# Kernel optimization log

Hardware: AMD Instinct MI355X
Metric: run time of the kernel (lower is better)

## Reference

```python
import jax, jax.numpy as jnp
import numpy as np

WEIGHT = 0.1
SELF_WEIGHT = 1.0
OTHER_WEIGHT = 1.0

def setup_inputs() -> dict:
    key = jax.random.key(0)
    k1, k2 = jax.random.split(key)
    B, D = 8192, 128
    output = jax.random.normal(k1, (B, D), dtype=jnp.float32)
    target = jax.random.normal(k2, (B, D), dtype=jnp.float32)
    return {"output": output, "target": target}

def reference(output, target):
    # Pairwise Euclidean distances d[i, n] = ||output[i] - target[n]||_2
    # no [B, B, D] intermediate).
    B = output.shape[0]
    xx = jnp.sum(output * output, axis=-1)          # [B]
    yy = jnp.sum(target * target, axis=-1)          # [B]
    d2 = xx[:, None] + yy[None, :] - 2.0 * (output @ target.T)  # [B, B]
    d = jnp.sqrt(jnp.maximum(d2, 0.0))
    diag_sum = jnp.trace(d)                          # sum of self distances
    total_sum = jnp.sum(d)
    other_sum = total_sum - diag_sum
    loss = (-diag_sum * SELF_WEIGHT + other_sum * OTHER_WEIGHT) / B * WEIGHT
    return loss
```

## Files before the change

### kernel.cpp

```cpp
#include <hip/hip_runtime.h>
#include <stdint.h>

typedef float f32x16 __attribute__((ext_vector_type(16)));
typedef int v8i __attribute__((ext_vector_type(8)));
typedef int v4i __attribute__((ext_vector_type(4)));

#define BDIM 8192


__global__ __launch_bounds__(256) void prep_kernel(const float* __restrict__ out_f,
                                                   const float* __restrict__ tgt_f,
                                                   uint8_t* __restrict__ ak,
                                                   float* __restrict__ xxyy) {
    const float* src = blockIdx.y ? tgt_f : out_f;
    uint8_t* dst = ak + (size_t)blockIdx.y * (1u << 20);
    float* nrm = xxyy + (size_t)blockIdx.y * BDIM;

    const int tid = threadIdx.x;
    const int lane = tid & 63;
    const int w = tid >> 6;
    const int jg = lane & 15;
    const int r = blockIdx.x * 16 + w * 4 + (lane >> 4);

    const float4* s4 = (const float4*)(src + (size_t)r * 128 + jg * 8);
    float4 a = s4[0], b = s4[1];

    uint32_t w0 = __builtin_amdgcn_cvt_pk_fp8_f32(a.x, a.y, 0, false);
    w0 = __builtin_amdgcn_cvt_pk_fp8_f32(a.z, a.w, w0, true);
    uint32_t w1 = __builtin_amdgcn_cvt_pk_fp8_f32(b.x, b.y, 0, false);
    w1 = __builtin_amdgcn_cvt_pk_fp8_f32(b.z, b.w, w1, true);

    *(uint2*)(dst + (jg >> 3) * 524288 + ((jg >> 2) & 1) * 262144
                  + ((jg >> 1) & 1) * 131072 + r * 16 + (jg & 1) * 8)
        = make_uint2(w0, w1);

    float sq = a.x*a.x + a.y*a.y + a.z*a.z + a.w*a.w
             + b.x*b.x + b.y*b.y + b.z*b.z + b.w*b.w;
    sq += __shfl_xor(sq, 1); sq += __shfl_xor(sq, 2);
    sq += __shfl_xor(sq, 4); sq += __shfl_xor(sq, 8);
    if (jg == 0) nrm[r] = sq;
}

__global__ __launch_bounds__(256, 4) void dist_kernel(const uint8_t* __restrict__ Ak,
                                                      const uint8_t* __restrict__ Bk,
                                                      const float* __restrict__ xxg,
                                                      const float* __restrict__ yyg,
                                                      float* __restrict__ partials) {
    __shared__ uint8_t sA[16384] __attribute__((aligned(16)));
    __shared__ uint8_t sB[16384] __attribute__((aligned(16)));
    __shared__ float xxl[128];
    __shared__ float yyl[128];
    __shared__ float wsum[4];

    const int tid = threadIdx.x;
    const int lane = tid & 63;
    const int wid = tid >> 6;
    const int wr = wid >> 1, wc = wid & 1;
    const int bx = blockIdx.x, by = blockIdx.y;

    {
        const int c0 = wid * 8;
        #pragma unroll
        for (int i = 0; i < 8; ++i) {
            int c = c0 + i;
            int mat = c >> 4, rem = c & 15, s = rem >> 1, half = rem & 1;
            int bidx = mat ? by : bx;
            const uint8_t* g = (mat ? Bk : Ak)
                + (s >> 2) * 524288 + ((s >> 1) & 1) * 262144 + (s & 1) * 131072
                + ((size_t)(bidx * 128 + half * 64)) * 16 + lane * 16;
            uint8_t* l = (mat ? sB : sA) + s * 2048 + half * 1024;
            __builtin_amdgcn_global_load_lds(
                (const __attribute__((address_space(1))) unsigned int*)g,
                (__attribute__((address_space(3))) unsigned int*)l, 16, 0, 0);
        }
    }
    if (tid < 128) xxl[tid] = xxg[bx * 128 + tid];
    else           yyl[tid - 128] = yyg[by * 128 + (tid - 128)];
    __syncthreads();

    const int lm = lane & 31;
    const int fh = lane >> 5;
    const v4i* A4 = (const v4i*)sA;
    const v4i* B4 = (const v4i*)sB;

    f32x16 acc[2][2] = {};
    #pragma unroll
    for (int S = 0; S < 2; ++S) {
        const int sb = S * 4 + fh * 2;
        v4i a0l = A4[(sb + 0) * 128 + wr * 64 + lm];
        v4i a0h = A4[(sb + 1) * 128 + wr * 64 + lm];
        v4i a1l = A4[(sb + 0) * 128 + wr * 64 + 32 + lm];
        v4i a1h = A4[(sb + 1) * 128 + wr * 64 + 32 + lm];
        v4i b0l = B4[(sb + 0) * 128 + wc * 64 + lm];
        v4i b0h = B4[(sb + 1) * 128 + wc * 64 + lm];
        v4i b1l = B4[(sb + 0) * 128 + wc * 64 + 32 + lm];
        v4i b1h = B4[(sb + 1) * 128 + wc * 64 + 32 + lm];
        v8i a0 = __builtin_shufflevector(a0l, a0h, 0, 1, 2, 3, 4, 5, 6, 7);
        v8i a1 = __builtin_shufflevector(a1l, a1h, 0, 1, 2, 3, 4, 5, 6, 7);
        v8i b0 = __builtin_shufflevector(b0l, b0h, 0, 1, 2, 3, 4, 5, 6, 7);
        v8i b1 = __builtin_shufflevector(b1l, b1h, 0, 1, 2, 3, 4, 5, 6, 7);
        acc[0][0] = __builtin_amdgcn_mfma_scale_f32_32x32x64_f8f6f4(
                        a0, b0, acc[0][0], 0, 0, 0, 0x7F7F7F7F, 0, 0x7F7F7F7F);
        acc[0][1] = __builtin_amdgcn_mfma_scale_f32_32x32x64_f8f6f4(
                        a0, b1, acc[0][1], 0, 0, 0, 0x7F7F7F7F, 0, 0x7F7F7F7F);
        acc[1][0] = __builtin_amdgcn_mfma_scale_f32_32x32x64_f8f6f4(
                        a1, b0, acc[1][0], 0, 0, 0, 0x7F7F7F7F, 0, 0x7F7F7F7F);
        acc[1][1] = __builtin_amdgcn_mfma_scale_f32_32x32x64_f8f6f4(
                        a1, b1, acc[1][1], 0, 0, 0, 0x7F7F7F7F, 0, 0x7F7F7F7F);
    }

    float s0 = 0.0f, s1 = 0.0f;
    #pragma unroll
    for (int tr = 0; tr < 2; ++tr) {
        float xv[16];
        #pragma unroll
        for (int q = 0; q < 4; ++q) {
            float4 t = *(const float4*)&xxl[wr * 64 + tr * 32 + 8 * q + 4 * fh];
            xv[q * 4 + 0] = t.x; xv[q * 4 + 1] = t.y;
            xv[q * 4 + 2] = t.z; xv[q * 4 + 3] = t.w;
        }
        #pragma unroll
        for (int tc = 0; tc < 2; ++tc) {
            float yv = yyl[wc * 64 + tc * 32 + lm];
            #pragma unroll
            for (int r = 0; r < 16; ++r) {
                float d2 = fmaf(-2.0f, acc[tr][tc][r], xv[r] + yv);
                float d = __builtin_amdgcn_sqrtf(__builtin_fabsf(d2));
                if (r & 1) s1 += d; else s0 += d;
            }
        }
    }
    float s = s0 + s1;

    if (bx == by && wr == wc) {
        #pragma unroll
        for (int t = 0; t < 2; ++t) {
            #pragma unroll
            for (int r = 0; r < 16; ++r) {
                int row = (r & 3) + 8 * (r >> 2) + 4 * fh;
                if (row == lm) {
                    int idx = wr * 64 + t * 32 + row;
                    float d2 = fmaf(-2.0f, acc[t][t][r], xxl[idx] + yyl[idx]);
                    s -= 2.0f * __builtin_amdgcn_sqrtf(__builtin_fabsf(d2));
                }
            }
        }
    }

    #pragma unroll
    for (int off = 32; off > 0; off >>= 1) s += __shfl_down(s, off);
    if (lane == 0) wsum[wid] = s;
    __syncthreads();
    if (tid == 0) partials[by * 64 + bx] = wsum[0] + wsum[1] + wsum[2] + wsum[3];
}

__global__ __launch_bounds__(256) void reduce_kernel(const float* __restrict__ partials,
                                                     float* __restrict__ out) {
    __shared__ float wsum[4];
    float s = 0.0f;
    #pragma unroll
    for (int i = 0; i < 16; ++i) s += partials[threadIdx.x + i * 256];
    #pragma unroll
    for (int off = 32; off > 0; off >>= 1) s += __shfl_down(s, off);
    int lane = threadIdx.x & 63, wid = threadIdx.x >> 6;
    if (lane == 0) wsum[wid] = s;
    __syncthreads();
    if (threadIdx.x == 0)
        out[0] = (wsum[0] + wsum[1] + wsum[2] + wsum[3]) * (0.1f / 8192.0f);
}

extern "C" void kernel_launch(void* const* d_in, const int* in_sizes, int n_in,
                              void* d_out, int out_size, void* d_ws, size_t ws_size,
                              hipStream_t stream) {
    const float* output = (const float*)d_in[0];
    const float* target = (const float*)d_in[1];

    uint8_t* ws = (uint8_t*)d_ws;
    uint8_t* ak      = ws;
    float*   xxyy    = (float*)(ws + (2u << 20));
    float*   partial = (float*)(ws + (2u << 20) + (64u << 10));

    prep_kernel<<<dim3(512, 2), 256, 0, stream>>>(output, target, ak, xxyy);
    dist_kernel<<<dim3(64, 64), 256, 0, stream>>>(ak, ak + (1u << 20),
                                                  xxyy, xxyy + BDIM, partial);
    reduce_kernel<<<1, 256, 0, stream>>>(partial, (float*)d_out);
}
```

Measured before the change: 78.58 us.

## Loop each block over four B tiles with double-buffered async LDS staging

Each distance block now keeps its A tile resident and iterates over four consecutive B column tiles. The next B tile and its norms are prefetched into a second LDS buffer while the current tile is computed. This amortizes the A load and launch cost and overlaps global-to-LDS transfers with MFMA work, cutting the grid from 4096 to 1024 blocks and the partial count to match. The costs are a larger LDS footprint (occupancy hint lowered to 3), fewer blocks to fill the GPU, and an extra barrier per iteration.

```diff
diff --git a/kernel.cpp b/kernel.cpp
--- a/kernel.cpp
+++ b/kernel.cpp
@@ -41,117 +41,148 @@
     if (jg == 0) nrm[r] = sq;
 }
 
-__global__ __launch_bounds__(256, 4) void dist_kernel(const uint8_t* __restrict__ Ak,
+__device__ __forceinline__ size_t seg_off(int s) {
+    return (size_t)(s >> 2) * 524288 + (size_t)((s >> 1) & 1) * 262144
+         + (size_t)(s & 1) * 131072;
+}
+
+__device__ __forceinline__ void stage_tile(const uint8_t* g0, int r0,
+                                           uint8_t* dst, int wid, int lane) {
+    #pragma unroll
+    for (int i = 0; i < 4; ++i) {
+        int c = wid * 4 + i;
+        int s = c >> 1, half = c & 1;
+        const uint8_t* g = g0 + seg_off(s) + (size_t)(r0 + half * 64 + lane) * 16;
+        uint8_t* l = dst + s * 2048 + half * 1024 + lane * 16;
+        __builtin_amdgcn_global_load_lds(
+            (const __attribute__((address_space(1))) unsigned int*)g,
+            (__attribute__((address_space(3))) unsigned int*)l, 16, 0, 0);
+    }
+}
+
+__device__ __forceinline__ void stage_f128(const float* g, float* l,
+                                           int wid, int wbase, int lane) {
+    if (wid == wbase || wid == wbase + 1) {
+        int half = wid - wbase;
+        __builtin_amdgcn_global_load_lds(
+            (const __attribute__((address_space(1))) unsigned int*)(g + half * 64 + lane),
+            (__attribute__((address_space(3))) unsigned int*)(l + half * 64 + lane), 4, 0, 0);
+    }
+}
+
+__global__ __launch_bounds__(256, 3) void dist_kernel(const uint8_t* __restrict__ Ak,
                                                       const uint8_t* __restrict__ Bk,
                                                       const float* __restrict__ xxg,
                                                       const float* __restrict__ yyg,
                                                       float* __restrict__ partials) {
     __shared__ uint8_t sA[16384] __attribute__((aligned(16)));
-    __shared__ uint8_t sB[16384] __attribute__((aligned(16)));
+    __shared__ uint8_t sB[2][16384] __attribute__((aligned(16)));
     __shared__ float xxl[128];
-    __shared__ float yyl[128];
+    __shared__ float yyl[2][128];
     __shared__ float wsum[4];
 
     const int tid = threadIdx.x;
     const int lane = tid & 63;
     const int wid = tid >> 6;
     const int wr = wid >> 1, wc = wid & 1;
-    const int bx = blockIdx.x, by = blockIdx.y;
-
-    {
-        const int c0 = wid * 8;
-        #pragma unroll
-        for (int i = 0; i < 8; ++i) {
-            int c = c0 + i;
-            int mat = c >> 4, rem = c & 15, s = rem >> 1, half = rem & 1;
-            int bidx = mat ? by : bx;
-            const uint8_t* g = (mat ? Bk : Ak)
-                + (s >> 2) * 524288 + ((s >> 1) & 1) * 262144 + (s & 1) * 131072
-                + ((size_t)(bidx * 128 + half * 64)) * 16 + lane * 16;
-            uint8_t* l = (mat ? sB : sA) + s * 2048 + half * 1024;
-            __builtin_amdgcn_global_load_lds(
-                (const __attribute__((address_space(1))) unsigned int*)g,
-                (__attribute__((address_space(3))) unsigned int*)l, 16, 0, 0);
-        }
-    }
-    if (tid < 128) xxl[tid] = xxg[bx * 128 + tid];
-    else           yyl[tid - 128] = yyg[by * 128 + (tid - 128)];
+    const int bx = blockIdx.x, byg = blockIdx.y;
+
+    stage_tile(Ak, bx * 128, sA, wid, lane);
+    stage_tile(Bk, byg * 512, sB[0], wid, lane);
+    stage_f128(xxg + bx * 128, xxl, wid, 2, lane);
+    stage_f128(yyg + byg * 512, yyl[0], wid, 0, lane);
     __syncthreads();
 
     const int lm = lane & 31;
     const int fh = lane >> 5;
     const v4i* A4 = (const v4i*)sA;
-    const v4i* B4 = (const v4i*)sB;
-
-    f32x16 acc[2][2] = {};
-    #pragma unroll
-    for (int S = 0; S < 2; ++S) {
-        const int sb = S * 4 + fh * 2;
-        v4i a0l = A4[(sb + 0) * 128 + wr * 64 + lm];
-        v4i a0h = A4[(sb + 1) * 128 + wr * 64 + lm];
-        v4i a1l = A4[(sb + 0) * 128 + wr * 64 + 32 + lm];
-        v4i a1h = A4[(sb + 1) * 128 + wr * 64 + 32 + lm];
-        v4i b0l = B4[(sb + 0) * 128 + wc * 64 + lm];
-        v4i b0h = B4[(sb + 1) * 128 + wc * 64 + lm];
-        v4i b1l = B4[(sb + 0) * 128 + wc * 64 + 32 + lm];
-        v4i b1h = B4[(sb + 1) * 128 + wc * 64 + 32 + lm];
-        v8i a0 = __builtin_shufflevector(a0l, a0h, 0, 1, 2, 3, 4, 5, 6, 7);
-        v8i a1 = __builtin_shufflevector(a1l, a1h, 0, 1, 2, 3, 4, 5, 6, 7);
-        v8i b0 = __builtin_shufflevector(b0l, b0h, 0, 1, 2, 3, 4, 5, 6, 7);
-        v8i b1 = __builtin_shufflevector(b1l, b1h, 0, 1, 2, 3, 4, 5, 6, 7);
-        acc[0][0] = __builtin_amdgcn_mfma_scale_f32_32x32x64_f8f6f4(
-                        a0, b0, acc[0][0], 0, 0, 0, 0x7F7F7F7F, 0, 0x7F7F7F7F);
-        acc[0][1] = __builtin_amdgcn_mfma_scale_f32_32x32x64_f8f6f4(
-                        a0, b1, acc[0][1], 0, 0, 0, 0x7F7F7F7F, 0, 0x7F7F7F7F);
-        acc[1][0] = __builtin_amdgcn_mfma_scale_f32_32x32x64_f8f6f4(
-                        a1, b0, acc[1][0], 0, 0, 0, 0x7F7F7F7F, 0, 0x7F7F7F7F);
-        acc[1][1] = __builtin_amdgcn_mfma_scale_f32_32x32x64_f8f6f4(
-                        a1, b1, acc[1][1], 0, 0, 0, 0x7F7F7F7F, 0, 0x7F7F7F7F);
-    }
-
-    float s0 = 0.0f, s1 = 0.0f;
-    #pragma unroll
-    for (int tr = 0; tr < 2; ++tr) {
-        float xv[16];
+
+    float xv[2][16];
+    #pragma unroll
+    for (int tr = 0; tr < 2; ++tr)
         #pragma unroll
         for (int q = 0; q < 4; ++q) {
             float4 t = *(const float4*)&xxl[wr * 64 + tr * 32 + 8 * q + 4 * fh];
-            xv[q * 4 + 0] = t.x; xv[q * 4 + 1] = t.y;
-            xv[q * 4 + 2] = t.z; xv[q * 4 + 3] = t.w;
-        }
+            xv[tr][q * 4 + 0] = t.x; xv[tr][q * 4 + 1] = t.y;
+            xv[tr][q * 4 + 2] = t.z; xv[tr][q * 4 + 3] = t.w;
+        }
+
+    float s0 = 0.0f, s1 = 0.0f;
+    float sdiag = 0.0f;
+
+    #pragma unroll
+    for (int j = 0; j < 4; ++j) {
+        const int cur = j & 1;
+        const int by = byg * 4 + j;
+
+        if (j < 3) {
+            stage_tile(Bk, (by + 1) * 128, sB[cur ^ 1], wid, lane);
+            stage_f128(yyg + (by + 1) * 128, yyl[cur ^ 1], wid, 0, lane);
+        }
+
+        const v4i* B4 = (const v4i*)sB[cur];
+        f32x16 acc[2][2] = {};
         #pragma unroll
-        for (int tc = 0; tc < 2; ++tc) {
-            float yv = yyl[wc * 64 + tc * 32 + lm];
+        for (int S = 0; S < 2; ++S) {
+            const int sb = S * 4 + fh * 2;
+            v4i a0l = A4[(sb + 0) * 128 + wr * 64 + lm];
+            v4i a0h = A4[(sb + 1) * 128 + wr * 64 + lm];
+            v4i a1l = A4[(sb + 0) * 128 + wr * 64 + 32 + lm];
+            v4i a1h = A4[(sb + 1) * 128 + wr * 64 + 32 + lm];
+            v4i b0l = B4[(sb + 0) * 128 + wc * 64 + lm];
+            v4i b0h = B4[(sb + 1) * 128 + wc * 64 + lm];
+            v4i b1l = B4[(sb + 0) * 128 + wc * 64 + 32 + lm];
+            v4i b1h = B4[(sb + 1) * 128 + wc * 64 + 32 + lm];
+            v8i a0 = __builtin_shufflevector(a0l, a0h, 0, 1, 2, 3, 4, 5, 6, 7);
+            v8i a1 = __builtin_shufflevector(a1l, a1h, 0, 1, 2, 3, 4, 5, 6, 7);
+            v8i b0 = __builtin_shufflevector(b0l, b0h, 0, 1, 2, 3, 4, 5, 6, 7);
+            v8i b1 = __builtin_shufflevector(b1l, b1h, 0, 1, 2, 3, 4, 5, 6, 7);
+            acc[0][0] = __builtin_amdgcn_mfma_scale_f32_32x32x64_f8f6f4(
+                            a0, b0, acc[0][0], 0, 0, 0, 0x7F7F7F7F, 0, 0x7F7F7F7F);
+            acc[0][1] = __builtin_amdgcn_mfma_scale_f32_32x32x64_f8f6f4(
+                            a0, b1, acc[0][1], 0, 0, 0, 0x7F7F7F7F, 0, 0x7F7F7F7F);
+            acc[1][0] = __builtin_amdgcn_mfma_scale_f32_32x32x64_f8f6f4(
+                            a1, b0, acc[1][0], 0, 0, 0, 0x7F7F7F7F, 0, 0x7F7F7F7F);
+            acc[1][1] = __builtin_amdgcn_mfma_scale_f32_32x32x64_f8f6f4(
+                            a1, b1, acc[1][1], 0, 0, 0, 0x7F7F7F7F, 0, 0x7F7F7F7F);
+        }
+
+        #pragma unroll
+        for (int tr = 0; tr < 2; ++tr)
             #pragma unroll
-            for (int r = 0; r < 16; ++r) {
-                float d2 = fmaf(-2.0f, acc[tr][tc][r], xv[r] + yv);
-                float d = __builtin_amdgcn_sqrtf(__builtin_fabsf(d2));
-                if (r & 1) s1 += d; else s0 += d;
-            }
-        }
-    }
-    float s = s0 + s1;
-
-    if (bx == by && wr == wc) {
-        #pragma unroll
-        for (int t = 0; t < 2; ++t) {
-            #pragma unroll
-            for (int r = 0; r < 16; ++r) {
-                int row = (r & 3) + 8 * (r >> 2) + 4 * fh;
-                if (row == lm) {
-                    int idx = wr * 64 + t * 32 + row;
-                    float d2 = fmaf(-2.0f, acc[t][t][r], xxl[idx] + yyl[idx]);
-                    s -= 2.0f * __builtin_amdgcn_sqrtf(__builtin_fabsf(d2));
+            for (int tc = 0; tc < 2; ++tc) {
+                float yv = yyl[cur][wc * 64 + tc * 32 + lm];
+                #pragma unroll
+                for (int r = 0; r < 16; ++r) {
+                    float d2 = fmaf(-2.0f, acc[tr][tc][r], xv[tr][r] + yv);
+                    float d = __builtin_amdgcn_sqrtf(__builtin_fabsf(d2));
+                    if (r & 1) s1 += d; else s0 += d;
                 }
             }
-        }
+
+        if (bx == by && wr == wc) {
+            #pragma unroll
+            for (int t = 0; t < 2; ++t)
+                #pragma unroll
+                for (int r = 0; r < 16; ++r) {
+                    int row = (r & 3) + 8 * (r >> 2) + 4 * fh;
+                    if (row == lm) {
+                        int idx = wr * 64 + t * 32 + row;
+                        float d2 = fmaf(-2.0f, acc[t][t][r], xxl[idx] + yyl[cur][idx]);
+                        sdiag += 2.0f * __builtin_amdgcn_sqrtf(__builtin_fabsf(d2));
+                    }
+                }
+        }
+
+        __syncthreads();
     }
 
+    float s = s0 + s1 - sdiag;
     #pragma unroll
     for (int off = 32; off > 0; off >>= 1) s += __shfl_down(s, off);
     if (lane == 0) wsum[wid] = s;
     __syncthreads();
-    if (tid == 0) partials[by * 64 + bx] = wsum[0] + wsum[1] + wsum[2] + wsum[3];
+    if (tid == 0) partials[byg * 64 + bx] = wsum[0] + wsum[1] + wsum[2] + wsum[3];
 }
 
 __global__ __launch_bounds__(256) void reduce_kernel(const float* __restrict__ partials,
@@ -159,7 +190,7 @@
     __shared__ float wsum[4];
     float s = 0.0f;
     #pragma unroll
-    for (int i = 0; i < 16; ++i) s += partials[threadIdx.x + i * 256];
+    for (int i = 0; i < 4; ++i) s += partials[threadIdx.x + i * 256];
     #pragma unroll
     for (int off = 32; off > 0; off >>= 1) s += __shfl_down(s, off);
     int lane = threadIdx.x & 63, wid = threadIdx.x >> 6;
@@ -181,7 +212,7 @@
     float*   partial = (float*)(ws + (2u << 20) + (64u << 10));
 
     prep_kernel<<<dim3(512, 2), 256, 0, stream>>>(output, target, ak, xxyy);
-    dist_kernel<<<dim3(64, 64), 256, 0, stream>>>(ak, ak + (1u << 20),
+    dist_kernel<<<dim3(64, 16), 256, 0, stream>>>(ak, ak + (1u << 20),
                                                   xxyy, xxyy + BDIM, partial);
     reduce_kernel<<<1, 256, 0, stream>>>(partial, (float*)d_out);
 }
```

Result: slower. 306.2 us (+289.6%).
